# Kernel optimization log

Hardware: AMD Instinct MI355X
Metric: run time of the kernel (lower is better)

Reference implementation:

```python
import jax, jax.numpy as jnp
import numpy as np

POOL = 7
IMAGE_SHAPE = (1024, 1024)
N_BOXES = 1000
B = 2
C = 256


def _make_boxes(key, n, batch):
    k1, k2, k3, k4 = jax.random.split(key, 4)
    bi = jax.random.randint(k1, (n,), 0, batch).astype(jnp.float32)
    # normalized [y1,x1,y2,x2] with sizes in [0.05,0.5] -> roi levels spread over 2..5
    c1 = jax.random.uniform(k2, (n, 2), minval=0.0, maxval=0.5)
    sz = jax.random.uniform(k3, (n, 2), minval=0.05, maxval=0.5)
    c2 = jnp.minimum(c1 + sz, 1.0)
    return jnp.concatenate([bi[:, None], c1[:, :1], c1[:, 1:], c2[:, :1], c2[:, 1:]], axis=1)


def setup_inputs() -> dict:
    key = jax.random.key(0)
    kb, k2, k3, k4, k5 = jax.random.split(key, 5)
    boxes = _make_boxes(kb, N_BOXES, B)
    f2 = jax.random.normal(k2, (B, C, 256, 256), dtype=jnp.float32)
    f3 = jax.random.normal(k3, (B, C, 128, 128), dtype=jnp.float32)
    f4 = jax.random.normal(k4, (B, C, 64, 64), dtype=jnp.float32)
    f5 = jax.random.normal(k5, (B, C, 32, 32), dtype=jnp.float32)
    return {"boxes": boxes, "f2": f2, "f3": f3, "f4": f4, "f5": f5}


def _roi_align(fmap, rois, bidx, scale, pool):
    """torchvision RoIAlign, aligned=False, sampling_ratio=0.
    rois: [N,4] as (x1,y1,x2,y2) in un-scaled coords (faithful to level_boxes=boxes[:,1:]).
    Since coords are normalized and scale<=1/4, roi dims clamp to 1.0 < pool, so the
    adaptive grid ceil(roi_dim/pool) == 1 sample per bin exactly."""
    H, W = fmap.shape[2], fmap.shape[3]
    x1 = rois[:, 0] * scale
    y1 = rois[:, 1] * scale
    x2 = rois[:, 2] * scale
    y2 = rois[:, 3] * scale
    rw = jnp.maximum(x2 - x1, 1.0)
    rh = jnp.maximum(y2 - y1, 1.0)
    bw = rw / pool
    bh = rh / pool
    p = jnp.arange(pool, dtype=jnp.float32) + 0.5
    ys = y1[:, None] + p[None, :] * bh[:, None]          # [N,P]
    xs = x1[:, None] + p[None, :] * bw[:, None]          # [N,P]
    n = rois.shape[0]
    y = jnp.broadcast_to(ys[:, :, None], (n, pool, pool))  # y varies over ph
    x = jnp.broadcast_to(xs[:, None, :], (n, pool, pool))  # x varies over pw
    valid = (y > -1.0) & (y < H) & (x > -1.0) & (x < W)
    yc = jnp.clip(y, 0.0, H - 1)
    xc = jnp.clip(x, 0.0, W - 1)
    y0 = jnp.floor(yc).astype(jnp.int32)
    x0 = jnp.floor(xc).astype(jnp.int32)
    y1i = jnp.minimum(y0 + 1, H - 1)
    x1i = jnp.minimum(x0 + 1, W - 1)
    ly = yc - y0.astype(jnp.float32)
    lx = xc - x0.astype(jnp.float32)
    hy = 1.0 - ly
    hx = 1.0 - lx
    bb = jnp.broadcast_to(bidx[:, None, None], (n, pool, pool))

    def g(yi, xi):
        return fmap[bb, :, yi, xi]  # [N,P,P,C]

    out = (
        (hy * hx)[..., None] * g(y0, x0)
        + (hy * lx)[..., None] * g(y0, x1i)
        + (ly * hx)[..., None] * g(y1i, x0)
        + (ly * lx)[..., None] * g(y1i, x1i)
    )
    out = jnp.where(valid[..., None], out, 0.0)
    return jnp.transpose(out, (0, 3, 1, 2))  # [N,C,P,P]


def reference(boxes, f2, f3, f4, f5):
    boxes = jax.lax.stop_gradient(boxes)  # original detaches level_boxes
    y1, x1, y2, x2 = boxes[:, 1], boxes[:, 2], boxes[:, 3], boxes[:, 4]
    h = y2 - y1
    w = x2 - x1
    image_area = float(IMAGE_SHAPE[0] * IMAGE_SHAPE[1])
    roi_level = 4.0 + jnp.log2(jnp.sqrt(h * w) / (224.0 / jnp.sqrt(jnp.float32(image_area))))
    roi_level = jnp.clip(jnp.round(roi_level).astype(jnp.int32), 2, 5)
    bidx = boxes[:, 0].astype(jnp.int32)
    rois = boxes[:, 1:]  # passed as (x1,y1,x2,y2) to RoIAlign, faithful to source
    feats = [f2, f3, f4, f5]
    pooled = jnp.stack(
        [_roi_align(feats[i], rois, bidx, 1.0 / 2 ** (i + 2), POOL) for i in range(4)],
        axis=0,
    )  # [4,N,C,P,P]
    n = boxes.shape[0]
    return pooled[roi_level - 2, jnp.arange(n)]  # [N,C,P,P], original box order
```

## Files before the change

### kernel.cpp

```cpp
#include <hip/hip_runtime.h>

#define POOL 7
#define NCH 256
#define NBOX 1000
#define PER_BOX (NCH * POOL * POOL)
#define TOTAL (NBOX * PER_BOX)
#define TOTAL4 (TOTAL / 4)

#define T2 0.0059814453125f
#define T3 0.02392578125f
#define T4 0.095703125f

__global__ __launch_bounds__(256) void pyramid_roialign_kernel(
    const float* __restrict__ boxes,
    const float* __restrict__ f2,
    const float* __restrict__ f3,
    const float* __restrict__ f4,
    const float* __restrict__ f5,
    float* __restrict__ out)
{
    unsigned gid = blockIdx.x * blockDim.x + threadIdx.x;
    if (gid >= TOTAL4) return;
    unsigned base = gid * 4u;
    unsigned n = base / PER_BOX;
    unsigned rem = base - n * PER_BOX;

    const float* bx = boxes + n * 5u;
    float b0 = bx[0];
    float r0 = bx[1], r1 = bx[2], r2 = bx[3], r3 = bx[4];

    float a = (r2 - r0) * (r3 - r1);
    int lvl = (a >= T2) + (a >= T3) + (a >= T4);

    const float* fmap = (lvl == 0) ? f2 : (lvl == 1) ? f3 : (lvl == 2) ? f4 : f5;
    int H = 256 >> lvl;
    const float scales[4] = {0.25f, 0.125f, 0.0625f, 0.03125f};
    float scale = scales[lvl];

    int bidx = (int)b0;

    float x1 = r0 * scale, y1 = r1 * scale;
    float x2 = r2 * scale, y2 = r3 * scale;
    float bw = fmaxf(x2 - x1, 1.0f) * (1.0f / POOL);
    float bh = fmaxf(y2 - y1, 1.0f) * (1.0f / POOL);

    float Hf = (float)H;
    float Hm1 = (float)(H - 1);
    unsigned planeStride = (unsigned)(H * H);
    unsigned batchOff = (unsigned)bidx * NCH * planeStride;

    float4 res;
    float* resp = &res.x;

    #pragma unroll
    for (int i = 0; i < 4; ++i) {
        unsigned e = rem + i;
        unsigned c = e / 49u;
        unsigned s = e - c * 49u;
        unsigned py = s / 7u;
        unsigned px = s - py * 7u;

        float y = y1 + ((float)py + 0.5f) * bh;
        float x = x1 + ((float)px + 0.5f) * bw;
        bool valid = (y > -1.0f) & (y < Hf) & (x > -1.0f) & (x < Hf);

        float yc = fminf(fmaxf(y, 0.0f), Hm1);
        float xc = fminf(fmaxf(x, 0.0f), Hm1);
        float y0f = floorf(yc);
        float x0f = floorf(xc);
        int y0 = (int)y0f;
        int x0 = (int)x0f;
        int y1i = min(y0 + 1, H - 1);
        int x1i = min(x0 + 1, H - 1);
        float ly = yc - y0f;
        float lx = xc - x0f;
        float hy = 1.0f - ly;
        float hx = 1.0f - lx;

        const float* plane = fmap + batchOff + c * planeStride;
        float v00 = plane[y0  * H + x0 ];
        float v01 = plane[y0  * H + x1i];
        float v10 = plane[y1i * H + x0 ];
        float v11 = plane[y1i * H + x1i];

        float r = (hy * hx) * v00 + (hy * lx) * v01 + (ly * hx) * v10 + (ly * lx) * v11;
        resp[i] = valid ? r : 0.0f;
    }

    *reinterpret_cast<float4*>(out + base) = res;
}

extern "C" void kernel_launch(void* const* d_in, const int* in_sizes, int n_in,
                              void* d_out, int out_size, void* d_ws, size_t ws_size,
                              hipStream_t stream) {
    const float* boxes = (const float*)d_in[0];
    const float* f2 = (const float*)d_in[1];
    const float* f3 = (const float*)d_in[2];
    const float* f4 = (const float*)d_in[3];
    const float* f5 = (const float*)d_in[4];
    float* out = (float*)d_out;

    int threads = 256;
    int blocks = (TOTAL4 + threads - 1) / threads;
    pyramid_roialign_kernel<<<blocks, threads, 0, stream>>>(boxes, f2, f3, f4, f5, out);
}
```

Before: 232.0 us.

## Compute one box per block with separable bilinear weights over a 3x3 patch

Each block now handles one box and each thread one channel. A thread loads only the first three rows of its feature plane as float4 vectors, builds separable x/y interpolation weights once, and evaluates all 49 bins as two small matrix contractions. Results are staged in shared memory and written out as coalesced float4 stores. This removes the per-element index math and the scattered four-point gathers. It relies on normalized box coordinates keeping every sample point inside the 3x3 corner of the map, and it uses about 49 KB of LDS per block, which caps occupancy.

```diff
diff --git a/kernel.cpp b/kernel.cpp
--- a/kernel.cpp
+++ b/kernel.cpp
@@ -4,12 +4,10 @@
 #define NCH 256
 #define NBOX 1000
 #define PER_BOX (NCH * POOL * POOL)
-#define TOTAL (NBOX * PER_BOX)
-#define TOTAL4 (TOTAL / 4)
 
-#define T2 0.0059814453125f
-#define T3 0.02392578125f
-#define T4 0.095703125f
+#define TL2 0.0059814453125f
+#define TL3 0.02392578125f
+#define TL4 0.095703125f
 
 __global__ __launch_bounds__(256) void pyramid_roialign_kernel(
     const float* __restrict__ boxes,
@@ -19,75 +17,103 @@
     const float* __restrict__ f5,
     float* __restrict__ out)
 {
-    unsigned gid = blockIdx.x * blockDim.x + threadIdx.x;
-    if (gid >= TOTAL4) return;
-    unsigned base = gid * 4u;
-    unsigned n = base / PER_BOX;
-    unsigned rem = base - n * PER_BOX;
+    __shared__ __align__(16) float outLds[PER_BOX];
 
-    const float* bx = boxes + n * 5u;
-    float b0 = bx[0];
-    float r0 = bx[1], r1 = bx[2], r2 = bx[3], r3 = bx[4];
+    const int n = blockIdx.x;
+    const int t = threadIdx.x;
 
-    float a = (r2 - r0) * (r3 - r1);
-    int lvl = (a >= T2) + (a >= T3) + (a >= T4);
+    const float* bx = boxes + n * 5;
+    const float b0 = bx[0];
+    const float r0 = bx[1], r1 = bx[2], r2 = bx[3], r3 = bx[4];
 
+    const float area = (r2 - r0) * (r3 - r1);
+    const int lvl = (area >= TL2) + (area >= TL3) + (area >= TL4);
     const float* fmap = (lvl == 0) ? f2 : (lvl == 1) ? f3 : (lvl == 2) ? f4 : f5;
-    int H = 256 >> lvl;
-    const float scales[4] = {0.25f, 0.125f, 0.0625f, 0.03125f};
-    float scale = scales[lvl];
+    const int H = 256 >> lvl;
+    const float scale = (lvl == 0) ? 0.25f : (lvl == 1) ? 0.125f
+                       : (lvl == 2) ? 0.0625f : 0.03125f;
 
-    int bidx = (int)b0;
+    const int bidx = (int)b0;
 
-    float x1 = r0 * scale, y1 = r1 * scale;
-    float x2 = r2 * scale, y2 = r3 * scale;
-    float bw = fmaxf(x2 - x1, 1.0f) * (1.0f / POOL);
-    float bh = fmaxf(y2 - y1, 1.0f) * (1.0f / POOL);
+    const float x1 = r0 * scale, y1 = r1 * scale;
+    const float x2 = r2 * scale, y2 = r3 * scale;
+    const float bw = fmaxf(x2 - x1, 1.0f) * (1.0f / POOL);
+    const float bh = fmaxf(y2 - y1, 1.0f) * (1.0f / POOL);
+    const float Hf = (float)H, Hm1 = (float)(H - 1);
 
-    float Hf = (float)H;
-    float Hm1 = (float)(H - 1);
-    unsigned planeStride = (unsigned)(H * H);
-    unsigned batchOff = (unsigned)bidx * NCH * planeStride;
+    const float* plane = fmap + ((size_t)bidx * NCH + (size_t)t) * (size_t)(H * H);
+    const float4 row0 = *reinterpret_cast<const float4*>(plane);
+    const float4 row1 = *reinterpret_cast<const float4*>(plane + H);
+    const float4 row2 = *reinterpret_cast<const float4*>(plane + 2 * H);
 
-    float4 res;
-    float* resp = &res.x;
-
+    float wx0[POOL], wx1[POOL], wx2[POOL];
+    float wy0[POOL], wy1[POOL], wy2[POOL];
     #pragma unroll
-    for (int i = 0; i < 4; ++i) {
-        unsigned e = rem + i;
-        unsigned c = e / 49u;
-        unsigned s = e - c * 49u;
-        unsigned py = s / 7u;
-        unsigned px = s - py * 7u;
-
-        float y = y1 + ((float)py + 0.5f) * bh;
-        float x = x1 + ((float)px + 0.5f) * bw;
-        bool valid = (y > -1.0f) & (y < Hf) & (x > -1.0f) & (x < Hf);
-
-        float yc = fminf(fmaxf(y, 0.0f), Hm1);
-        float xc = fminf(fmaxf(x, 0.0f), Hm1);
-        float y0f = floorf(yc);
-        float x0f = floorf(xc);
-        int y0 = (int)y0f;
-        int x0 = (int)x0f;
-        int y1i = min(y0 + 1, H - 1);
-        int x1i = min(x0 + 1, H - 1);
-        float ly = yc - y0f;
-        float lx = xc - x0f;
-        float hy = 1.0f - ly;
-        float hx = 1.0f - lx;
-
-        const float* plane = fmap + batchOff + c * planeStride;
-        float v00 = plane[y0  * H + x0 ];
-        float v01 = plane[y0  * H + x1i];
-        float v10 = plane[y1i * H + x0 ];
-        float v11 = plane[y1i * H + x1i];
-
-        float r = (hy * hx) * v00 + (hy * lx) * v01 + (ly * hx) * v10 + (ly * lx) * v11;
-        resp[i] = valid ? r : 0.0f;
+    for (int p = 0; p < POOL; ++p) {
+        const float pc = (float)p + 0.5f;
+        {
+            float x = x1 + pc * bw;
+            bool ok = (x > -1.0f) && (x < Hf);
+            float xc = fminf(fmaxf(x, 0.0f), Hm1);
+            float x0f = floorf(xc);
+            float lx = xc - x0f;
+            float hx = 1.0f - lx;
+            bool sel = x0f >= 0.5f;
+            float w0 = sel ? 0.0f : hx;
+            float w1 = sel ? hx : lx;
+            float w2 = sel ? lx : 0.0f;
+            wx0[p] = ok ? w0 : 0.0f;
+            wx1[p] = ok ? w1 : 0.0f;
+            wx2[p] = ok ? w2 : 0.0f;
+        }
+        {
+            float y = y1 + pc * bh;
+            bool ok = (y > -1.0f) && (y < Hf);
+            float yc = fminf(fmaxf(y, 0.0f), Hm1);
+            float y0f = floorf(yc);
+            float ly = yc - y0f;
+            float hy = 1.0f - ly;
+            bool sel = y0f >= 0.5f;
+            float w0 = sel ? 0.0f : hy;
+            float w1 = sel ? hy : ly;
+            float w2 = sel ? ly : 0.0f;
+            wy0[p] = ok ? w0 : 0.0f;
+            wy1[p] = ok ? w1 : 0.0f;
+            wy2[p] = ok ? w2 : 0.0f;
+        }
     }
 
-    *reinterpret_cast<float4*>(out + base) = res;
+    float Ty0[POOL], Ty1[POOL], Ty2[POOL];
+    #pragma unroll
+    for (int p = 0; p < POOL; ++p) {
+        Ty0[p] = wx0[p] * row0.x + wx1[p] * row0.y + wx2[p] * row0.z;
+        Ty1[p] = wx0[p] * row1.x + wx1[p] * row1.y + wx2[p] * row1.z;
+        Ty2[p] = wx0[p] * row2.x + wx1[p] * row2.y + wx2[p] * row2.z;
+    }
+
+    float* myLds = outLds + t * 49;
+    #pragma unroll
+    for (int py = 0; py < POOL; ++py) {
+        #pragma unroll
+        for (int px = 0; px < POOL; ++px) {
+            myLds[py * 7 + px] =
+                wy0[py] * Ty0[px] + wy1[py] * Ty1[px] + wy2[py] * Ty2[px];
+        }
+    }
+    __syncthreads();
+
+    float* ob = out + (size_t)n * PER_BOX;
+    #pragma unroll
+    for (int k = 0; k < 12; ++k) {
+        int e = 4 * (t + 256 * k);
+        float4 v = *reinterpret_cast<const float4*>(outLds + e);
+        *reinterpret_cast<float4*>(ob + e) = v;
+    }
+    if (t < 64) {
+        int e = 4 * (t + 3072);
+        float4 v = *reinterpret_cast<const float4*>(outLds + e);
+        *reinterpret_cast<float4*>(ob + e) = v;
+    }
 }
 
 extern "C" void kernel_launch(void* const* d_in, const int* in_sizes, int n_in,
@@ -100,7 +126,5 @@
     const float* f5 = (const float*)d_in[4];
     float* out = (float*)d_out;
 
-    int threads = 256;
-    int blocks = (TOTAL4 + threads - 1) / threads;
-    pyramid_roialign_kernel<<<blocks, threads, 0, stream>>>(boxes, f2, f3, f4, f5, out);
+    pyramid_roialign_kernel<<<NBOX, 256, 0, stream>>>(boxes, f2, f3, f4, f5, out);
 }
```

After: 201.8 us. -13.0%, faster.
